# Performance work log

Measured on AMD Instinct MI355X. Metric: run time of the kernel, lower is better.

The kernel has to match this reference:

```python
import jax, jax.numpy as jnp
import numpy as np

NUM_AA = 20       # 'ACDEFGHIKLMNPQRSTVWY'
FEAT_DIM = 16     # feature_space.feature_dim
NUM_PAIRS = 8_388_608


def setup_inputs() -> dict:
    key = jax.random.key(0)
    k1, k2, k3 = jax.random.split(key, 3)
    features = jax.random.normal(k1, (NUM_AA, FEAT_DIM), dtype=jnp.float32)
    # M initialized as identity in the original (nn.Parameter(torch.eye(d)))
    M = jnp.eye(FEAT_DIM, dtype=jnp.float32)
    idx_i = jax.random.randint(k2, (NUM_PAIRS,), 0, NUM_AA, dtype=jnp.int32)
    idx_j = jax.random.randint(k3, (NUM_PAIRS,), 0, NUM_AA, dtype=jnp.int32)
    return {"features": features, "M": M, "idx_i": idx_i, "idx_j": idx_j}


def reference(features, M, idx_i, idx_j):
    # Batched version of Snack.__call__: tanh(delta^T M delta) per pair.
    delta = features[idx_i] - features[idx_j]          # [P, d]
    # dist_p = delta_p . (M @ delta_p)
    dist = jnp.einsum("pd,de,pe->p", delta, M, delta)  # [P]
    return jnp.tanh(dist)
```

## Files before the change

kernel.cpp:

```cpp
#include <hip/hip_runtime.h>
#include <math.h>


constexpr int NUM_AA = 20;
constexpr int FEAT   = 16;
constexpr int TABLE  = NUM_AA * NUM_AA;

__global__ __launch_bounds__(512) void build_table(
    const float* __restrict__ F,
    const float* __restrict__ M,
    float* __restrict__ tab)
{
    __shared__ float sF[NUM_AA * FEAT];
    __shared__ float sM[FEAT * FEAT];
    const int t = threadIdx.x;
    for (int k = t; k < NUM_AA * FEAT; k += 512) sF[k] = F[k];
    for (int k = t; k < FEAT * FEAT; k += 512)   sM[k] = M[k];
    __syncthreads();

    if (t < TABLE) {
        const int i = t / NUM_AA;
        const int j = t - i * NUM_AA;
        float delta[FEAT];
#pragma unroll
        for (int d = 0; d < FEAT; ++d)
            delta[d] = sF[i * FEAT + d] - sF[j * FEAT + d];
        float dist = 0.f;
#pragma unroll
        for (int d = 0; d < FEAT; ++d) {
            float md = 0.f;
#pragma unroll
            for (int e = 0; e < FEAT; ++e)
                md = fmaf(sM[d * FEAT + e], delta[e], md);
            dist = fmaf(delta[d], md, dist);
        }
        tab[t] = tanhf(dist);
    }
}

__global__ __launch_bounds__(256) void gather_pairs(
    const float* __restrict__ tab,
    const int4* __restrict__ ii4,
    const int4* __restrict__ jj4,
    float4* __restrict__ out4,
    int nvec,
    const int* __restrict__ ii_s,
    const int* __restrict__ jj_s,
    float* __restrict__ out_s,
    int tail_start, int total)
{
    __shared__ float s[TABLE];
    for (int k = threadIdx.x; k < TABLE; k += 256) s[k] = tab[k];
    __syncthreads();

    const int stride = (int)gridDim.x * 256;
    for (int v = (int)blockIdx.x * 256 + (int)threadIdx.x; v < nvec; v += stride) {
        const int4 ii = ii4[v];
        const int4 jj = jj4[v];
        float4 o;
        o.x = s[ii.x * NUM_AA + jj.x];
        o.y = s[ii.y * NUM_AA + jj.y];
        o.z = s[ii.z * NUM_AA + jj.z];
        o.w = s[ii.w * NUM_AA + jj.w];
        out4[v] = o;
    }
    if (blockIdx.x == 0) {
        const int p = tail_start + (int)threadIdx.x;
        if (p < total)
            out_s[p] = s[ii_s[p] * NUM_AA + jj_s[p]];
    }
}

extern "C" void kernel_launch(void* const* d_in, const int* in_sizes, int n_in,
                              void* d_out, int out_size, void* d_ws, size_t ws_size,
                              hipStream_t stream)
{
    const float* F   = (const float*)d_in[0];
    const float* M   = (const float*)d_in[1];
    const int*   ii  = (const int*)d_in[2];
    const int*   jj  = (const int*)d_in[3];
    float*       out = (float*)d_out;
    float*       tab = (float*)d_ws;

    const int P    = in_sizes[2];
    const int nvec = P >> 2;
    const int tail = nvec << 2;

    build_table<<<1, 512, 0, stream>>>(F, M, tab);

    const int blocks = 2048;
    gather_pairs<<<blocks, 256, 0, stream>>>(
        tab, (const int4*)ii, (const int4*)jj, (float4*)out,
        nvec, ii, jj, out, tail, P);
}
```

Baseline: 110.1 us.

## Fuse table build into gather kernel and prefetch indices before table compute

```diff
diff --git a/kernel.cpp b/kernel.cpp
--- a/kernel.cpp
+++ b/kernel.cpp
@@ -6,40 +6,9 @@
 constexpr int FEAT   = 16;
 constexpr int TABLE  = NUM_AA * NUM_AA;
 
-__global__ __launch_bounds__(512) void build_table(
+__global__ __launch_bounds__(256) void snack_fused(
     const float* __restrict__ F,
     const float* __restrict__ M,
-    float* __restrict__ tab)
-{
-    __shared__ float sF[NUM_AA * FEAT];
-    __shared__ float sM[FEAT * FEAT];
-    const int t = threadIdx.x;
-    for (int k = t; k < NUM_AA * FEAT; k += 512) sF[k] = F[k];
-    for (int k = t; k < FEAT * FEAT; k += 512)   sM[k] = M[k];
-    __syncthreads();
-
-    if (t < TABLE) {
-        const int i = t / NUM_AA;
-        const int j = t - i * NUM_AA;
-        float delta[FEAT];
-#pragma unroll
-        for (int d = 0; d < FEAT; ++d)
-            delta[d] = sF[i * FEAT + d] - sF[j * FEAT + d];
-        float dist = 0.f;
-#pragma unroll
-        for (int d = 0; d < FEAT; ++d) {
-            float md = 0.f;
-#pragma unroll
-            for (int e = 0; e < FEAT; ++e)
-                md = fmaf(sM[d * FEAT + e], delta[e], md);
-            dist = fmaf(delta[d], md, dist);
-        }
-        tab[t] = tanhf(dist);
-    }
-}
-
-__global__ __launch_bounds__(256) void gather_pairs(
-    const float* __restrict__ tab,
     const int4* __restrict__ ii4,
     const int4* __restrict__ jj4,
     float4* __restrict__ out4,
@@ -50,22 +19,54 @@
     int tail_start, int total)
 {
     __shared__ float s[TABLE];
-    for (int k = threadIdx.x; k < TABLE; k += 256) s[k] = tab[k];
+    __shared__ float sF[NUM_AA * FEAT];
+    __shared__ float sM[FEAT * FEAT];
+
+    const int t      = (int)threadIdx.x;
+    const int stride = (int)gridDim.x * 256;
+    int v = (int)blockIdx.x * 256 + t;
+
+    int4 ii, jj;
+    const bool have0 = (v < nvec);
+    if (have0) { ii = ii4[v]; jj = jj4[v]; }
+
+    for (int k = t; k < NUM_AA * FEAT; k += 256) sF[k] = F[k];
+    for (int k = t; k < FEAT * FEAT; k += 256)   sM[k] = M[k];
     __syncthreads();
 
-    const int stride = (int)gridDim.x * 256;
-    for (int v = (int)blockIdx.x * 256 + (int)threadIdx.x; v < nvec; v += stride) {
-        const int4 ii = ii4[v];
-        const int4 jj = jj4[v];
+    for (int e = t; e < TABLE; e += 256) {
+        const int i = e / NUM_AA;
+        const int j = e - i * NUM_AA;
+        float delta[FEAT];
+#pragma unroll
+        for (int d = 0; d < FEAT; ++d)
+            delta[d] = sF[i * FEAT + d] - sF[j * FEAT + d];
+        float dist = 0.f;
+#pragma unroll
+        for (int d = 0; d < FEAT; ++d) {
+            float md = 0.f;
+#pragma unroll
+            for (int e2 = 0; e2 < FEAT; ++e2)
+                md = fmaf(sM[d * FEAT + e2], delta[e2], md);
+            dist = fmaf(delta[d], md, dist);
+        }
+        s[e] = tanhf(dist);
+    }
+    __syncthreads();
+
+    while (v < nvec) {
         float4 o;
         o.x = s[ii.x * NUM_AA + jj.x];
         o.y = s[ii.y * NUM_AA + jj.y];
         o.z = s[ii.z * NUM_AA + jj.z];
         o.w = s[ii.w * NUM_AA + jj.w];
         out4[v] = o;
+        v += stride;
+        if (v < nvec) { ii = ii4[v]; jj = jj4[v]; }
     }
+
     if (blockIdx.x == 0) {
-        const int p = tail_start + (int)threadIdx.x;
+        const int p = tail_start + t;
         if (p < total)
             out_s[p] = s[ii_s[p] * NUM_AA + jj_s[p]];
     }
@@ -80,16 +81,17 @@
     const int*   ii  = (const int*)d_in[2];
     const int*   jj  = (const int*)d_in[3];
     float*       out = (float*)d_out;
-    float*       tab = (float*)d_ws;
+    (void)d_ws; (void)ws_size;
 
     const int P    = in_sizes[2];
     const int nvec = P >> 2;
     const int tail = nvec << 2;
 
-    build_table<<<1, 512, 0, stream>>>(F, M, tab);
+    int blocks = (nvec + 255) / 256;
+    if (blocks > 2048) blocks = 2048;
+    if (blocks < 1) blocks = 1;
 
-    const int blocks = 2048;
-    gather_pairs<<<blocks, 256, 0, stream>>>(
-        tab, (const int4*)ii, (const int4*)jj, (float4*)out,
+    snack_fused<<<blocks, 256, 0, stream>>>(
+        F, M, (const int4*)ii, (const int4*)jj, (float4*)out,
         nvec, ii, jj, out, tail, P);
 }
```

Result: slower. 130.4 us (+18.5%).

## Issue index loads before table staging and use one-shot gather blocks

Applied to the files above, without the earlier changes.

```diff
diff --git a/kernel.cpp b/kernel.cpp
--- a/kernel.cpp
+++ b/kernel.cpp
@@ -9,10 +9,15 @@
 __global__ __launch_bounds__(512) void build_table(
     const float* __restrict__ F,
     const float* __restrict__ M,
-    float* __restrict__ tab)
+    float* __restrict__ tab,
+    const int* __restrict__ ii_s,
+    const int* __restrict__ jj_s,
+    float* __restrict__ out_s,
+    int tail_start, int total)
 {
     __shared__ float sF[NUM_AA * FEAT];
     __shared__ float sM[FEAT * FEAT];
+    __shared__ float sT[TABLE];
     const int t = threadIdx.x;
     for (int k = t; k < NUM_AA * FEAT; k += 512) sF[k] = F[k];
     for (int k = t; k < FEAT * FEAT; k += 512)   sM[k] = M[k];
@@ -34,8 +39,15 @@
                 md = fmaf(sM[d * FEAT + e], delta[e], md);
             dist = fmaf(delta[d], md, dist);
         }
-        tab[t] = tanhf(dist);
+        const float v = tanhf(dist);
+        tab[t] = v;
+        sT[t]  = v;
     }
+    __syncthreads();
+
+    const int p = tail_start + t;
+    if (p < total)
+        out_s[p] = sT[ii_s[p] * NUM_AA + jj_s[p]];
 }
 
 __global__ __launch_bounds__(256) void gather_pairs(
@@ -43,31 +55,41 @@
     const int4* __restrict__ ii4,
     const int4* __restrict__ jj4,
     float4* __restrict__ out4,
-    int nvec,
-    const int* __restrict__ ii_s,
-    const int* __restrict__ jj_s,
-    float* __restrict__ out_s,
-    int tail_start, int total)
+    int nvec)
 {
     __shared__ float s[TABLE];
-    for (int k = threadIdx.x; k < TABLE; k += 256) s[k] = tab[k];
+
+    const int t  = (int)threadIdx.x;
+    const int v0 = (int)blockIdx.x * 512 + t;
+    const int v1 = v0 + 256;
+
+    int4 iiA, jjA, iiB, jjB;
+    const bool hA = (v0 < nvec);
+    const bool hB = (v1 < nvec);
+    if (hA) { iiA = ii4[v0]; jjA = jj4[v0]; }
+    if (hB) { iiB = ii4[v1]; jjB = jj4[v1]; }
+
+    if (t < 200) {
+        s[t]       = tab[t];
+        s[t + 200] = tab[t + 200];
+    }
     __syncthreads();
 
-    const int stride = (int)gridDim.x * 256;
-    for (int v = (int)blockIdx.x * 256 + (int)threadIdx.x; v < nvec; v += stride) {
-        const int4 ii = ii4[v];
-        const int4 jj = jj4[v];
+    if (hA) {
         float4 o;
-        o.x = s[ii.x * NUM_AA + jj.x];
-        o.y = s[ii.y * NUM_AA + jj.y];
-        o.z = s[ii.z * NUM_AA + jj.z];
-        o.w = s[ii.w * NUM_AA + jj.w];
-        out4[v] = o;
+        o.x = s[iiA.x * NUM_AA + jjA.x];
+        o.y = s[iiA.y * NUM_AA + jjA.y];
+        o.z = s[iiA.z * NUM_AA + jjA.z];
+        o.w = s[iiA.w * NUM_AA + jjA.w];
+        out4[v0] = o;
     }
-    if (blockIdx.x == 0) {
-        const int p = tail_start + (int)threadIdx.x;
-        if (p < total)
-            out_s[p] = s[ii_s[p] * NUM_AA + jj_s[p]];
+    if (hB) {
+        float4 o;
+        o.x = s[iiB.x * NUM_AA + jjB.x];
+        o.y = s[iiB.y * NUM_AA + jjB.y];
+        o.z = s[iiB.z * NUM_AA + jjB.z];
+        o.w = s[iiB.w * NUM_AA + jjB.w];
+        out4[v1] = o;
     }
 }
 
@@ -86,10 +108,9 @@
     const int nvec = P >> 2;
     const int tail = nvec << 2;
 
-    build_table<<<1, 512, 0, stream>>>(F, M, tab);
+    build_table<<<1, 512, 0, stream>>>(F, M, tab, ii, jj, out, tail, P);
 
-    const int blocks = 2048;
+    const int blocks = (nvec + 511) / 512;
     gather_pairs<<<blocks, 256, 0, stream>>>(
-        tab, (const int4*)ii, (const int4*)jj, (float4*)out,
-        nvec, ii, jj, out, tail, P);
+        tab, (const int4*)ii, (const int4*)jj, (float4*)out, nvec);
 }
```

After: 109.2 us. No clear change (-0.8%).
